# Optimization experiments

Hardware: AMD Instinct MI355X
Metric: run time of the kernel (lower is better)

Reference implementation:

```python
import jax, jax.numpy as jnp
import numpy as np

NH = 6
D = 78  # dim_k = dim_v, dk = dv = 13 per head
SCALE = 1.0 / np.sqrt(D // NH).astype(np.float32)


def _split(t):
    # (B, n, D) -> (B, H, n, dk)
    B, n, d = t.shape
    return t.reshape(B, n, NH, d // NH).transpose(0, 2, 1, 3)


def _merge(t):
    # (B, H, n, dk) -> (B, n, D)
    B, h, n, d = t.shape
    return t.transpose(0, 2, 1, 3).reshape(B, n, h * d)


def _cross_attn(x, y, Wq, Wk, Wv):
    # MultiHeadCrossSelfAttention / MultiHeadSelfAttention math (dropout=identity in eval;
    # attn_mask is expanded but never applied in the original forward).
    q = _split(x @ Wq)
    k = _split(y @ Wk)
    v = _split(y @ Wv)
    dist = jax.nn.softmax(jnp.einsum('bhqd,bhkd->bhqk', q, k) * SCALE, axis=-1)
    return _merge(jnp.einsum('bhqk,bhkd->bhqd', dist, v))


def _contrastive_attn(x, y, Wq, Wk, Wv):
    # MultiHeadContrastiveSelfAttention: softmax -> (1 - p) -> softmax -> matmul, residual q add.
    q = _split(x @ Wq)
    k = _split(y @ Wk)
    v = _split(y @ Wv)
    dist = jax.nn.softmax(jnp.einsum('bhqd,bhkd->bhqk', q, k) * SCALE, axis=-1)
    dist = jax.nn.softmax(1.0 - dist, axis=-1)
    return _merge(q + jnp.einsum('bhqk,bhkd->bhqd', dist, v))


def setup_inputs() -> dict:
    key = jax.random.key(0)
    ks = jax.random.split(key, 20)
    B, nT, nV, nA = 8, 1024, 1024, 1024
    inp = {
        'x': jax.random.normal(ks[0], (B, nT, D), jnp.float32),
        'y': jax.random.normal(ks[1], (B, nV, D), jnp.float32),
        'z': jax.random.normal(ks[2], (B, nA, D), jnp.float32),
        'mask_tv': jnp.zeros((B, nT, nV), jnp.bool_),
        'mask_ta': jnp.zeros((B, nT, nA), jnp.bool_),
    }
    names = ['Wq_tv', 'Wk_tv', 'Wv_tv', 'Wq_ta', 'Wk_ta', 'Wv_ta',
             'Wq_ctv', 'Wk_ctv', 'Wv_ctv', 'Wq_cta', 'Wk_cta', 'Wv_cta',
             'Wq_s', 'Wk_s', 'Wv_s']
    for i, nm in enumerate(names):
        inp[nm] = jax.random.normal(ks[3 + i], (D, D), jnp.float32) * 0.05
    return inp


def reference(x, y, z, mask_tv, mask_ta,
              Wq_tv, Wk_tv, Wv_tv, Wq_ta, Wk_ta, Wv_ta,
              Wq_ctv, Wk_ctv, Wv_ctv, Wq_cta, Wk_cta, Wv_cta,
              Wq_s, Wk_s, Wv_s):
    # masks are dead args in the original module (expanded but never applied)
    att_tv = _cross_attn(x, y, Wq_tv, Wk_tv, Wv_tv)          # MHSCA_TV
    att_ta = _cross_attn(x, z, Wq_ta, Wk_ta, Wv_ta)          # MHSCA_TA
    c_tv = _contrastive_attn(x, y, Wq_ctv, Wk_ctv, Wv_ctv)   # MHSCTA_TV
    c_ta = _contrastive_attn(x, z, Wq_cta, Wk_cta, Wv_cta)   # MHSCTA_TA
    # fuse three pooled modality tokens through the length-3 MHSA
    tokens = jnp.stack([x.mean(axis=1),
                        (att_tv + c_tv).mean(axis=1),
                        (att_ta + c_ta).mean(axis=1)], axis=1)  # (B, 3, D)
    fused = _cross_attn(tokens, tokens, Wq_s, Wk_s, Wv_s)       # MHSA
    # (B, 4*1024 + 3, D)
    return jnp.concatenate([att_tv, c_tv, att_ta, c_ta, fused], axis=1)
```

## Files before the change

### kernel.cpp

```cpp
#include <hip/hip_runtime.h>
#include <hip/hip_bf16.h>

#define BB 8
#define NN 1024
#define DM 78
#define NH 6
#define DK 13
#define NROW 4099
#define QSCL 0.40013158f
#define SCALE 0.27735009811261457f
#define INV1023 0.000977517106549365f

using bf16 = __hip_bfloat16;
typedef __attribute__((ext_vector_type(8))) short short8;
typedef __attribute__((ext_vector_type(4))) float f32x4;

#if __has_builtin(__builtin_amdgcn_exp2f)
#define EXP2(x) __builtin_amdgcn_exp2f(x)
#else
__device__ __forceinline__ float EXP2(float x) {
    float r;
    asm volatile("v_exp_f32 %0, %1\n\ts_nop 1" : "=v"(r) : "v"(x));
    return r;
}
#endif

#define MATSZ ((size_t)48 * 1024 * 16)

struct PW { const float* w[12]; };

__device__ __forceinline__ unsigned pkbf2(float a, float b) {
    __hip_bfloat162 t = __float22bfloat162_rn(make_float2(a, b));
    return *(unsigned*)&t;
}

__global__ __launch_bounds__(320) void proj_kernel(const float* __restrict__ x,
                                                   const float* __restrict__ y,
                                                   const float* __restrict__ z,
                                                   PW p,
                                                   unsigned* __restrict__ Qbf,
                                                   unsigned* __restrict__ Kbf,
                                                   unsigned* __restrict__ Vt,
                                                   float* __restrict__ Qf32,
                                                   float* __restrict__ sv,
                                                   float* __restrict__ tok) {
    __shared__ float AT[78 * 68];
    __shared__ float WL[78 * 80];
    int bid = blockIdx.x;
    int mat = bid >> 7;
    int rb = bid & 127;
    const float* src = (mat < 4) ? x : (((mat - 4) & 1) ? z : y);
    int tid = threadIdx.x;
    const float* sp = src + (size_t)rb * 64 * DM;
    for (int i = tid; i < 64 * DM; i += 320) {
        int r = i / DM, e = i - r * DM;
        AT[e * 68 + r] = sp[i];
    }
    const float* W = p.w[mat];
    for (int i = tid; i < DM * DM; i += 320) {
        int e = i / DM, c = i - e * DM;
        WL[e * 80 + c] = W[i];
    }
    __syncthreads();
    int rowg = tid / 20, colg = tid % 20;
    float acc[4][4] = {{0.f}};
    for (int e = 0; e < DM; ++e) {
        float4 a = *(const float4*)&AT[e * 68 + rowg * 4];
        float4 w = *(const float4*)&WL[e * 80 + colg * 4];
        acc[0][0] = fmaf(a.x, w.x, acc[0][0]); acc[0][1] = fmaf(a.x, w.y, acc[0][1]);
        acc[0][2] = fmaf(a.x, w.z, acc[0][2]); acc[0][3] = fmaf(a.x, w.w, acc[0][3]);
        acc[1][0] = fmaf(a.y, w.x, acc[1][0]); acc[1][1] = fmaf(a.y, w.y, acc[1][1]);
        acc[1][2] = fmaf(a.y, w.z, acc[1][2]); acc[1][3] = fmaf(a.y, w.w, acc[1][3]);
        acc[2][0] = fmaf(a.z, w.x, acc[2][0]); acc[2][1] = fmaf(a.z, w.y, acc[2][1]);
        acc[2][2] = fmaf(a.z, w.z, acc[2][2]); acc[2][3] = fmaf(a.z, w.w, acc[2][3]);
        acc[3][0] = fmaf(a.w, w.x, acc[3][0]); acc[3][1] = fmaf(a.w, w.y, acc[3][1]);
        acc[3][2] = fmaf(a.w, w.z, acc[3][2]); acc[3][3] = fmaf(a.w, w.w, acc[3][3]);
    }
    __syncthreads();
    float* CT = WL;
#pragma unroll
    for (int j = 0; j < 4; ++j)
#pragma unroll
        for (int k = 0; k < 4; ++k) {
            int c = colg * 4 + k;
            if (c < DM) CT[(rowg * 4 + j) * 81 + c] = acc[j][k];
        }
    __syncthreads();
    int bb = rb >> 4;
    int i0 = (rb & 15) * 64;
    if (mat < 8) {
        unsigned* dst = (mat < 4) ? Qbf : Kbf;
        int m4 = (mat < 4) ? mat : mat - 4;
        float scl = (mat < 4) ? QSCL : 1.0f;
        for (int t2 = tid; t2 < NH * 64 * 8; t2 += 320) {
            int hh = t2 >> 9;
            int rem = t2 & 511;
            int r = rem >> 3, cp = rem & 7;
            int c0 = cp * 2, c1 = cp * 2 + 1;
            float a = (c0 < DK) ? CT[r * 81 + hh * DK + c0] * scl : 0.f;
            float bv = (c1 < DK) ? CT[r * 81 + hh * DK + c1] * scl : 0.f;
            dst[(((size_t)m4 * 48 + bb * NH + hh) * 1024 + i0 + r) * 8 + cp] = pkbf2(a, bv);
        }
        if (mat >= 2) {
            for (int t2 = tid; t2 < 64 * DM; t2 += 320) {
                int r = t2 / DM, c = t2 - r * DM;
                int hh = c / DK, dd = c - hh * DK;
                Qf32[((size_t)(mat - 2) * 48 + bb * NH + hh) * 1024 * DK +
                     (size_t)(i0 + r) * DK + dd] = CT[r * 81 + c];
            }
        }
    } else {
        for (int t2 = tid; t2 < NH * 16 * 32; t2 += 320) {
            int hh = t2 >> 9;
            int rem = t2 & 511;
            int dd = rem >> 5, cp = rem & 31;
            float a, bv;
            if (dd < DK) {
                a = CT[(cp * 2) * 81 + hh * DK + dd];
                bv = CT[(cp * 2 + 1) * 81 + hh * DK + dd];
            } else if (dd == 13) { a = 1.f; bv = 1.f; }
            else { a = 0.f; bv = 0.f; }
            Vt[(((size_t)(mat - 8) * 48 + bb * NH + hh) * 16 + dd) * 512 +
               (i0 >> 1) + cp] = pkbf2(a, bv);
        }
        if (mat >= 10 && tid < DM) {
            int hh = tid / DK, dd = tid - hh * DK;
            float s = 0.f;
            for (int r = 0; r < 64; ++r) s += CT[r * 81 + tid];
            atomicAdd(&sv[((size_t)(mat - 10) * 48 + bb * NH + hh) * DK + dd], s);
        }
    }
    if (mat == 0 && tid < DM) {
        float s = 0.f;
        for (int r = 0; r < 64; ++r) s += AT[tid * 68 + r];
        atomicAdd(&tok[bb * DM + tid], s);
    }
}

__global__ __launch_bounds__(256) void att_kernel(const bf16* __restrict__ Qbf,
                                                  const bf16* __restrict__ Kbf,
                                                  const bf16* __restrict__ Vt,
                                                  const float* __restrict__ Qf32,
                                                  const float* __restrict__ sv,
                                                  float* __restrict__ tok,
                                                  float* __restrict__ out) {
    __shared__ short PL[4 * 2560];
    int bid = blockIdx.x;
    int qt = bid & 7;
    int rest = bid >> 3;
    int h = rest % NH; rest /= NH;
    int b = rest & 7;
    int g = rest >> 3;
    int tid = threadIdx.x, wave = tid >> 6, lane = tid & 63;
    int quad = lane >> 4, lq = lane & 15;
    size_t mb = (size_t)g * 48 + b * NH + h;
    int q0 = qt * 64 + wave * 16;
    int q1 = q0 + 512;

    short8 zero8 = {0, 0, 0, 0, 0, 0, 0, 0};
    short8 qfA = zero8, qfB = zero8;
    if (quad < 2) {
        qfA = *(const short8*)((const short*)Qbf + (mb * 1024 + q0 + lq) * 16 + quad * 8);
        qfB = *(const short8*)((const short*)Qbf + (mb * 1024 + q1 + lq) * 16 + quad * 8);
    }
    const short* Kp = (const short*)Kbf + mb * 1024 * 16;
    const short* Vp = (const short*)Vt + mb * 16 * 1024 + (size_t)lq * 1024;
    short* myP = &PL[wave * 2560];
    f32x4 OA = {0.f, 0.f, 0.f, 0.f};
    f32x4 OB = {0.f, 0.f, 0.f, 0.f};
    const f32x4 zz = {0.f, 0.f, 0.f, 0.f};

    short8 kX0 = zero8, kX1 = zero8, kY0 = zero8, kY1 = zero8, vX, vY;
    if (quad < 2) {
        kX0 = *(const short8*)(Kp + lq * 16 + quad * 8);
        kX1 = *(const short8*)(Kp + (16 + lq) * 16 + quad * 8);
        kY0 = *(const short8*)(Kp + (32 + lq) * 16 + quad * 8);
        kY1 = *(const short8*)(Kp + (48 + lq) * 16 + quad * 8);
    }
    vX = *(const short8*)(Vp + quad * 8);
    vY = *(const short8*)(Vp + 32 + quad * 8);

    for (int kt = 0; kt < 16; ++kt) {
        int nkey = kt * 64 + 64;
        f32x4 SX0 = __builtin_amdgcn_mfma_f32_16x16x32_bf16(kX0, qfA, zz, 0, 0, 0);
        f32x4 SX1 = __builtin_amdgcn_mfma_f32_16x16x32_bf16(kX1, qfA, zz, 0, 0, 0);
        f32x4 SX2 = __builtin_amdgcn_mfma_f32_16x16x32_bf16(kX0, qfB, zz, 0, 0, 0);
        f32x4 SX3 = __builtin_amdgcn_mfma_f32_16x16x32_bf16(kX1, qfB, zz, 0, 0, 0);
        f32x4 SY0 = __builtin_amdgcn_mfma_f32_16x16x32_bf16(kY0, qfA, zz, 0, 0, 0);
        f32x4 SY1 = __builtin_amdgcn_mfma_f32_16x16x32_bf16(kY1, qfA, zz, 0, 0, 0);
        f32x4 SY2 = __builtin_amdgcn_mfma_f32_16x16x32_bf16(kY0, qfB, zz, 0, 0, 0);
        f32x4 SY3 = __builtin_amdgcn_mfma_f32_16x16x32_bf16(kY1, qfB, zz, 0, 0, 0);
        short8 kX0n = zero8, kX1n = zero8, kY0n = zero8, kY1n = zero8, vXn, vYn;
        if (quad < 2) {
            kX0n = *(const short8*)(Kp + (nkey + lq) * 16 + quad * 8);
            kX1n = *(const short8*)(Kp + (nkey + 16 + lq) * 16 + quad * 8);
            kY0n = *(const short8*)(Kp + (nkey + 32 + lq) * 16 + quad * 8);
            kY1n = *(const short8*)(Kp + (nkey + 48 + lq) * 16 + quad * 8);
        }
        vXn = *(const short8*)(Vp + nkey + quad * 8);
        vYn = *(const short8*)(Vp + nkey + 32 + quad * 8);

        uint2 w0, w1;
        w0.x = pkbf2(EXP2(SX0[0]), EXP2(SX0[1]));
        w0.y = pkbf2(EXP2(SX0[2]), EXP2(SX0[3]));
        w1.x = pkbf2(EXP2(SX1[0]), EXP2(SX1[1]));
        w1.y = pkbf2(EXP2(SX1[2]), EXP2(SX1[3]));
        *(uint2*)(myP + lq * 40 + quad * 4) = w0;
        *(uint2*)(myP + lq * 40 + 16 + quad * 4) = w1;
        w0.x = pkbf2(EXP2(SX2[0]), EXP2(SX2[1]));
        w0.y = pkbf2(EXP2(SX2[2]), EXP2(SX2[3]));
        w1.x = pkbf2(EXP2(SX3[0]), EXP2(SX3[1]));
        w1.y = pkbf2(EXP2(SX3[2]), EXP2(SX3[3]));
        *(uint2*)(myP + 640 + lq * 40 + quad * 4) = w0;
        *(uint2*)(myP + 640 + lq * 40 + 16 + quad * 4) = w1;
        w0.x = pkbf2(EXP2(SY0[0]), EXP2(SY0[1]));
        w0.y = pkbf2(EXP2(SY0[2]), EXP2(SY0[3]));
        w1.x = pkbf2(EXP2(SY1[0]), EXP2(SY1[1]));
        w1.y = pkbf2(EXP2(SY1[2]), EXP2(SY1[3]));
        *(uint2*)(myP + 1280 + lq * 40 + quad * 4) = w0;
        *(uint2*)(myP + 1280 + lq * 40 + 16 + quad * 4) = w1;
        w0.x = pkbf2(EXP2(SY2[0]), EXP2(SY2[1]));
        w0.y = pkbf2(EXP2(SY2[2]), EXP2(SY2[3]));
        w1.x = pkbf2(EXP2(SY3[0]), EXP2(SY3[1]));
        w1.y = pkbf2(EXP2(SY3[2]), EXP2(SY3[3]));
        *(uint2*)(myP + 1920 + lq * 40 + quad * 4) = w0;
        *(uint2*)(myP + 1920 + lq * 40 + 16 + quad * 4) = w1;
        asm volatile("s_waitcnt lgkmcnt(0)" ::: "memory");
        short8 pXA = *(const short8*)(myP + lq * 40 + quad * 8);
        short8 pXB = *(const short8*)(myP + 640 + lq * 40 + quad * 8);
        short8 pYA = *(const short8*)(myP + 1280 + lq * 40 + quad * 8);
        short8 pYB = *(const short8*)(myP + 1920 + lq * 40 + quad * 8);
        OA = __builtin_amdgcn_mfma_f32_16x16x32_bf16(pXA, vX, OA, 0, 0, 0);
        OB = __builtin_amdgcn_mfma_f32_16x16x32_bf16(pXB, vX, OB, 0, 0, 0);
        OA = __builtin_amdgcn_mfma_f32_16x16x32_bf16(pYA, vY, OA, 0, 0, 0);
        OB = __builtin_amdgcn_mfma_f32_16x16x32_bf16(pYB, vY, OB, 0, 0, 0);
        kX0 = kX0n; kX1 = kX1n; kY0 = kY0n; kY1 = kY1n; vX = vXn; vY = vYn;
    }

    size_t rowbase = (g == 0) ? 0 : (g == 1 ? 2 * NN : (g == 2 ? NN : 3 * NN));
    float lA[4], lB[4];
#pragma unroll
    for (int r = 0; r < 4; ++r) {
        lA[r] = __shfl(OA[r], (lane & 48) | 13, 64);
        lB[r] = __shfl(OB[r], (lane & 48) | 13, 64);
    }
    float svv = 0.f;
    const float* qf32p = nullptr;
    if (g >= 2) {
        if (lq < DK) svv = sv[((size_t)(g - 2) * 48 + b * NH + h) * DK + lq];
        qf32p = Qf32 + ((size_t)(g - 2) * 48 + b * NH + h) * 1024 * DK + lq;
    }
    float vsum = 0.f;
#pragma unroll
    for (int r = 0; r < 4; ++r) {
        int mA = q0 + quad * 4 + r;
        int mB = q1 + quad * 4 + r;
        float A0 = OA[r] / lA[r];
        float A1 = OB[r] / lB[r];
        float v0, v1;
        if (g < 2) { v0 = A0; v1 = A1; }
        else {
            float qr0 = (lq < DK) ? qf32p[(size_t)mA * DK] : 0.f;
            float qr1 = (lq < DK) ? qf32p[(size_t)mB * DK] : 0.f;
            v0 = qr0 + (svv - A0) * INV1023;
            v1 = qr1 + (svv - A1) * INV1023;
        }
        if (lq < DK) {
            out[((size_t)b * NROW + rowbase + mA) * DM + h * DK + lq] = v0;
            out[((size_t)b * NROW + rowbase + mB) * DM + h * DK + lq] = v1;
            vsum += v0 + v1;
        }
    }
    vsum += __shfl_xor(vsum, 16);
    vsum += __shfl_xor(vsum, 32);
    if (quad == 0 && lq < DK) {
        int tki = (g & 1) ? 2 : 1;
        atomicAdd(&tok[(size_t)tki * (8 * DM) + b * DM + h * DK + lq], vsum);
    }
}

__global__ __launch_bounds__(256) void fused_kernel(const float* __restrict__ tok,
                                                    const float* __restrict__ Wq,
                                                    const float* __restrict__ Wk,
                                                    const float* __restrict__ Wv,
                                                    float* __restrict__ out) {
    __shared__ float T[3 * DM], Qs[3 * DM], Ks[3 * DM], Vs[3 * DM], P[NH * 9];
    int b = blockIdx.x, tid = threadIdx.x;
    if (tid < 234) {
        int t = tid / DM, d = tid - t * DM;
        T[tid] = tok[(size_t)t * (8 * DM) + b * DM + d] * (1.f / NN);
    }
    __syncthreads();
    for (int idx = tid; idx < 702; idx += 256) {
        int mat = idx / 234;
        int rem = idx - mat * 234;
        int t = rem / DM, d = rem - t * DM;
        const float* W = (mat == 0) ? Wq : (mat == 1 ? Wk : Wv);
        float a = 0.f;
        for (int e = 0; e < DM; ++e) a = fmaf(T[t * DM + e], W[(size_t)e * DM + d], a);
        float* dst = (mat == 0) ? Qs : (mat == 1 ? Ks : Vs);
        dst[t * DM + d] = a;
    }
    __syncthreads();
    if (tid < NH * 3) {
        int h = tid / 3, t = tid % 3;
        float s[3];
        for (int k = 0; k < 3; ++k) {
            float a = 0.f;
            for (int d2 = 0; d2 < DK; ++d2)
                a += Qs[t * DM + h * DK + d2] * Ks[k * DM + h * DK + d2];
            s[k] = a * SCALE;
        }
        float mm = fmaxf(s[0], fmaxf(s[1], s[2]));
        float e0 = __expf(s[0] - mm), e1 = __expf(s[1] - mm), e2 = __expf(s[2] - mm);
        float inv = 1.f / (e0 + e1 + e2);
        P[(h * 3 + t) * 3 + 0] = e0 * inv;
        P[(h * 3 + t) * 3 + 1] = e1 * inv;
        P[(h * 3 + t) * 3 + 2] = e2 * inv;
    }
    __syncthreads();
    if (tid < 234) {
        int t = tid / DM, d = tid - t * DM, h = d / DK;
        float a = 0.f;
        for (int k = 0; k < 3; ++k) a += P[(h * 3 + t) * 3 + k] * Vs[k * DM + d];
        out[((size_t)b * NROW + 4 * NN + t) * DM + d] = a;
    }
}

extern "C" void kernel_launch(void* const* d_in, const int* in_sizes, int n_in,
                              void* d_out, int out_size, void* d_ws, size_t ws_size,
                              hipStream_t stream) {
    const float* bigs[3] = {nullptr, nullptr, nullptr};
    const float* w[15];
    int nb = 0, nw = 0;
    for (int i = 0; i < n_in; ++i) {
        if (in_sizes[i] == BB * NN * DM && nb < 3) bigs[nb++] = (const float*)d_in[i];
        else if (in_sizes[i] == DM * DM && nw < 15) w[nw++] = (const float*)d_in[i];
    }
    if (nb < 3 || nw < 15) {
        bigs[0] = (const float*)d_in[0]; bigs[1] = (const float*)d_in[1];
        bigs[2] = (const float*)d_in[2];
        int base = (n_in >= 20) ? 5 : 3;
        for (int i = 0; i < 15; ++i) w[i] = (const float*)d_in[base + i];
    }
    const float* x = bigs[0];
    const float* y = bigs[1];
    const float* z = bigs[2];
    float* out = (float*)d_out;

    bf16* Qbf = (bf16*)d_ws;
    bf16* Kbf = Qbf + 4 * MATSZ;
    bf16* Vt  = Kbf + 4 * MATSZ;
    float* Qf32 = (float*)(Vt + 4 * MATSZ);
    float* sv = Qf32 + (size_t)2 * 48 * 1024 * DK;
    float* tok = sv + 2 * 48 * DK;

    PW pp;
    const float* wsel[12] = {w[0], w[3], w[6], w[9],
                             w[1], w[4], w[7], w[10],
                             w[2], w[5], w[8], w[11]};
    for (int i = 0; i < 12; ++i) pp.w[i] = wsel[i];

    hipMemsetAsync(sv, 0, (2 * 48 * DK + 3 * 8 * DM) * sizeof(float), stream);
    proj_kernel<<<1536, 320, 0, stream>>>(x, y, z, pp, (unsigned*)Qbf, (unsigned*)Kbf,
                                          (unsigned*)Vt, Qf32, sv, tok);
    att_kernel<<<4 * BB * NH * 8, 256, 0, stream>>>(Qbf, Kbf, Vt, Qf32, sv, tok, out);
    fused_kernel<<<BB, 256, 0, stream>>>(tok, w[12], w[13], w[14], out);
}
```

Measured before the change: 220.8 us.

## Use bf16 MFMA for projections whose outputs are stored as bf16

The projection kernel is split into two paths. Blocks whose outputs are consumed only as bf16 (Q for the plain cross attention, K, V) now run a bf16 MFMA 16x16x32 GEMM on padded LDS tiles. The contrastive Q projections, which also need fp32 output for the residual add, keep an FP32 FMA path that now uses 256 threads and loads K in two chunks to shrink LDS. The aim is to cut projection compute time and LDS footprint so more blocks fit per CU, at the cost of bf16 input rounding in the GEMM and more complex block remapping.

```diff
diff --git a/kernel.cpp b/kernel.cpp
--- a/kernel.cpp
+++ b/kernel.cpp
@@ -34,7 +34,7 @@
     return *(unsigned*)&t;
 }
 
-__global__ __launch_bounds__(320) void proj_kernel(const float* __restrict__ x,
+__global__ __launch_bounds__(256) void proj_kernel(const float* __restrict__ x,
                                                    const float* __restrict__ y,
                                                    const float* __restrict__ z,
                                                    PW p,
@@ -44,96 +44,172 @@
                                                    float* __restrict__ Qf32,
                                                    float* __restrict__ sv,
                                                    float* __restrict__ tok) {
-    __shared__ float AT[78 * 68];
-    __shared__ float WL[78 * 80];
+    __shared__ unsigned SMEM[7488];
     int bid = blockIdx.x;
-    int mat = bid >> 7;
-    int rb = bid & 127;
+    int tid = threadIdx.x;
+    int mat, rb;
+    if (bid < 256) { mat = 2 + (bid >> 7); rb = bid & 127; }
+    else {
+        int t = bid - 256;
+        int midx = t >> 7;
+        mat = (midx < 2) ? midx : midx + 2;
+        rb = t & 127;
+    }
     const float* src = (mat < 4) ? x : (((mat - 4) & 1) ? z : y);
-    int tid = threadIdx.x;
     const float* sp = src + (size_t)rb * 64 * DM;
-    for (int i = tid; i < 64 * DM; i += 320) {
-        int r = i / DM, e = i - r * DM;
-        AT[e * 68 + r] = sp[i];
-    }
     const float* W = p.w[mat];
-    for (int i = tid; i < DM * DM; i += 320) {
-        int e = i / DM, c = i - e * DM;
-        WL[e * 80 + c] = W[i];
-    }
-    __syncthreads();
-    int rowg = tid / 20, colg = tid % 20;
-    float acc[4][4] = {{0.f}};
-    for (int e = 0; e < DM; ++e) {
-        float4 a = *(const float4*)&AT[e * 68 + rowg * 4];
-        float4 w = *(const float4*)&WL[e * 80 + colg * 4];
-        acc[0][0] = fmaf(a.x, w.x, acc[0][0]); acc[0][1] = fmaf(a.x, w.y, acc[0][1]);
-        acc[0][2] = fmaf(a.x, w.z, acc[0][2]); acc[0][3] = fmaf(a.x, w.w, acc[0][3]);
-        acc[1][0] = fmaf(a.y, w.x, acc[1][0]); acc[1][1] = fmaf(a.y, w.y, acc[1][1]);
-        acc[1][2] = fmaf(a.y, w.z, acc[1][2]); acc[1][3] = fmaf(a.y, w.w, acc[1][3]);
-        acc[2][0] = fmaf(a.z, w.x, acc[2][0]); acc[2][1] = fmaf(a.z, w.y, acc[2][1]);
-        acc[2][2] = fmaf(a.z, w.z, acc[2][2]); acc[2][3] = fmaf(a.z, w.w, acc[2][3]);
-        acc[3][0] = fmaf(a.w, w.x, acc[3][0]); acc[3][1] = fmaf(a.w, w.y, acc[3][1]);
-        acc[3][2] = fmaf(a.w, w.z, acc[3][2]); acc[3][3] = fmaf(a.w, w.w, acc[3][3]);
-    }
-    __syncthreads();
-    float* CT = WL;
-#pragma unroll
-    for (int j = 0; j < 4; ++j)
-#pragma unroll
-        for (int k = 0; k < 4; ++k) {
-            int c = colg * 4 + k;
-            if (c < DM) CT[(rowg * 4 + j) * 81 + c] = acc[j][k];
-        }
-    __syncthreads();
     int bb = rb >> 4;
     int i0 = (rb & 15) * 64;
-    if (mat < 8) {
-        unsigned* dst = (mat < 4) ? Qbf : Kbf;
-        int m4 = (mat < 4) ? mat : mat - 4;
-        float scl = (mat < 4) ? QSCL : 1.0f;
-        for (int t2 = tid; t2 < NH * 64 * 8; t2 += 320) {
+    float* CT = (float*)SMEM;
+
+    if (bid < 256) {
+        float* AT = (float*)SMEM;
+        float* WL = AT + 39 * 68;
+        int rowg = tid >> 4, colg = tid & 15;
+        float acc[4][5] = {{0.f}};
+        for (int ch = 0; ch < 2; ++ch) {
+            int e0 = ch * 39;
+            if (ch) __syncthreads();
+            for (int i = tid; i < 64 * 39; i += 256) {
+                int r = i / 39, er = i - r * 39;
+                AT[er * 68 + r] = sp[r * DM + e0 + er];
+            }
+            for (int i = tid; i < 39 * 80; i += 256) {
+                int er = i / 80, c = i - er * 80;
+                WL[er * 80 + c] = (c < DM) ? W[(size_t)(e0 + er) * DM + c] : 0.f;
+            }
+            __syncthreads();
+            if (mat == 2 && tid < 39) {
+                float s = 0.f;
+                for (int r = 0; r < 64; ++r) s += AT[tid * 68 + r];
+                atomicAdd(&tok[bb * DM + e0 + tid], s);
+            }
+            for (int er = 0; er < 39; ++er) {
+                float4 a4 = *(const float4*)&AT[er * 68 + rowg * 4];
+                float av[4] = {a4.x, a4.y, a4.z, a4.w};
+                const float* wr = &WL[er * 80 + colg * 5];
+                float w0 = wr[0], w1 = wr[1], w2 = wr[2], w3 = wr[3], w4 = wr[4];
+#pragma unroll
+                for (int j = 0; j < 4; ++j) {
+                    acc[j][0] = fmaf(av[j], w0, acc[j][0]);
+                    acc[j][1] = fmaf(av[j], w1, acc[j][1]);
+                    acc[j][2] = fmaf(av[j], w2, acc[j][2]);
+                    acc[j][3] = fmaf(av[j], w3, acc[j][3]);
+                    acc[j][4] = fmaf(av[j], w4, acc[j][4]);
+                }
+            }
+        }
+        __syncthreads();
+#pragma unroll
+        for (int j = 0; j < 4; ++j)
+#pragma unroll
+            for (int k = 0; k < 5; ++k) {
+                int c = colg * 5 + k;
+                if (c < DM) CT[(rowg * 4 + j) * 81 + c] = acc[j][k];
+            }
+        __syncthreads();
+        for (int t2 = tid; t2 < NH * 64 * 8; t2 += 256) {
             int hh = t2 >> 9;
             int rem = t2 & 511;
             int r = rem >> 3, cp = rem & 7;
             int c0 = cp * 2, c1 = cp * 2 + 1;
-            float a = (c0 < DK) ? CT[r * 81 + hh * DK + c0] * scl : 0.f;
-            float bv = (c1 < DK) ? CT[r * 81 + hh * DK + c1] * scl : 0.f;
-            dst[(((size_t)m4 * 48 + bb * NH + hh) * 1024 + i0 + r) * 8 + cp] = pkbf2(a, bv);
-        }
-        if (mat >= 2) {
-            for (int t2 = tid; t2 < 64 * DM; t2 += 320) {
-                int r = t2 / DM, c = t2 - r * DM;
-                int hh = c / DK, dd = c - hh * DK;
-                Qf32[((size_t)(mat - 2) * 48 + bb * NH + hh) * 1024 * DK +
-                     (size_t)(i0 + r) * DK + dd] = CT[r * 81 + c];
-            }
+            float a = (c0 < DK) ? CT[r * 81 + hh * DK + c0] * QSCL : 0.f;
+            float bv = (c1 < DK) ? CT[r * 81 + hh * DK + c1] * QSCL : 0.f;
+            Qbf[(((size_t)mat * 48 + bb * NH + hh) * 1024 + i0 + r) * 8 + cp] = pkbf2(a, bv);
+        }
+        for (int t2 = tid; t2 < 64 * DM; t2 += 256) {
+            int r = t2 / DM, c = t2 - r * DM;
+            int hh = c / DK, dd = c - hh * DK;
+            Qf32[((size_t)(mat - 2) * 48 + bb * NH + hh) * 1024 * DK +
+                 (size_t)(i0 + r) * DK + dd] = CT[r * 81 + c];
         }
     } else {
-        for (int t2 = tid; t2 < NH * 16 * 32; t2 += 320) {
-            int hh = t2 >> 9;
-            int rem = t2 & 511;
-            int dd = rem >> 5, cp = rem & 31;
-            float a, bv;
-            if (dd < DK) {
-                a = CT[(cp * 2) * 81 + hh * DK + dd];
-                bv = CT[(cp * 2 + 1) * 81 + hh * DK + dd];
-            } else if (dd == 13) { a = 1.f; bv = 1.f; }
-            else { a = 0.f; bv = 0.f; }
-            Vt[(((size_t)(mat - 8) * 48 + bb * NH + hh) * 16 + dd) * 512 +
-               (i0 >> 1) + cp] = pkbf2(a, bv);
-        }
-        if (mat >= 10 && tid < DM) {
-            int hh = tid / DK, dd = tid - hh * DK;
-            float s = 0.f;
-            for (int r = 0; r < 64; ++r) s += CT[r * 81 + tid];
-            atomicAdd(&sv[((size_t)(mat - 10) * 48 + bb * NH + hh) * DK + dd], s);
-        }
-    }
-    if (mat == 0 && tid < DM) {
-        float s = 0.f;
-        for (int r = 0; r < 64; ++r) s += AT[tid * 68 + r];
-        atomicAdd(&tok[bb * DM + tid], s);
+        unsigned* ALu = SMEM;
+        unsigned* WTu = SMEM + 64 * 52;
+        const float2* sp2 = (const float2*)sp;
+        for (int i = tid; i < 64 * 39; i += 256) {
+            float2 f2 = sp2[i];
+            int r = i / 39, pc = i - r * 39;
+            ALu[r * 52 + pc] = pkbf2(f2.x, f2.y);
+        }
+        for (int i = tid; i < 64 * 13; i += 256) {
+            int r = i / 13, pc = i - r * 13;
+            ALu[r * 52 + 39 + pc] = 0u;
+        }
+        for (int i = tid; i < 80 * 52; i += 256) {
+            int n = i / 52, pc = i - n * 52;
+            int k0 = pc * 2;
+            float a = (n < DM && k0 < DM) ? W[(size_t)k0 * DM + n] : 0.f;
+            float bv = (n < DM && k0 + 1 < DM) ? W[(size_t)(k0 + 1) * DM + n] : 0.f;
+            WTu[i] = pkbf2(a, bv);
+        }
+        __syncthreads();
+        int wv = tid >> 6, lane = tid & 63, quad = lane >> 4, lq = lane & 15;
+        int r0 = wv * 16;
+        const short* ALs = (const short*)ALu;
+        const short* WTs = (const short*)WTu;
+        short8 af0 = *(const short8*)(ALs + (r0 + lq) * 104 + quad * 8);
+        short8 af1 = *(const short8*)(ALs + (r0 + lq) * 104 + 32 + quad * 8);
+        short8 af2 = *(const short8*)(ALs + (r0 + lq) * 104 + 64 + quad * 8);
+        const f32x4 zz = {0.f, 0.f, 0.f, 0.f};
+        f32x4 acc[5];
+#pragma unroll
+        for (int n = 0; n < 5; ++n) acc[n] = zz;
+#pragma unroll
+        for (int n = 0; n < 5; ++n) {
+            const short* wb = WTs + (n * 16 + lq) * 104 + quad * 8;
+            acc[n] = __builtin_amdgcn_mfma_f32_16x16x32_bf16(
+                af0, *(const short8*)wb, acc[n], 0, 0, 0);
+            acc[n] = __builtin_amdgcn_mfma_f32_16x16x32_bf16(
+                af1, *(const short8*)(wb + 32), acc[n], 0, 0, 0);
+            acc[n] = __builtin_amdgcn_mfma_f32_16x16x32_bf16(
+                af2, *(const short8*)(wb + 64), acc[n], 0, 0, 0);
+        }
+        __syncthreads();
+#pragma unroll
+        for (int n = 0; n < 5; ++n) {
+            int c = n * 16 + lq;
+            if (c < DM) {
+#pragma unroll
+                for (int r = 0; r < 4; ++r)
+                    CT[(r0 + quad * 4 + r) * 81 + c] = acc[n][r];
+            }
+        }
+        __syncthreads();
+        if (mat < 8) {
+            unsigned* dst = (mat < 4) ? Qbf : Kbf;
+            int m4 = (mat < 4) ? mat : mat - 4;
+            float scl = (mat < 4) ? QSCL : 1.0f;
+            for (int t2 = tid; t2 < NH * 64 * 8; t2 += 256) {
+                int hh = t2 >> 9;
+                int rem = t2 & 511;
+                int r = rem >> 3, cp = rem & 7;
+                int c0 = cp * 2, c1 = cp * 2 + 1;
+                float a = (c0 < DK) ? CT[r * 81 + hh * DK + c0] * scl : 0.f;
+                float bv = (c1 < DK) ? CT[r * 81 + hh * DK + c1] * scl : 0.f;
+                dst[(((size_t)m4 * 48 + bb * NH + hh) * 1024 + i0 + r) * 8 + cp] = pkbf2(a, bv);
+            }
+        } else {
+            for (int t2 = tid; t2 < NH * 16 * 32; t2 += 256) {
+                int hh = t2 >> 9;
+                int rem = t2 & 511;
+                int dd = rem >> 5, cp = rem & 31;
+                float a, bv;
+                if (dd < DK) {
+                    a = CT[(cp * 2) * 81 + hh * DK + dd];
+                    bv = CT[(cp * 2 + 1) * 81 + hh * DK + dd];
+                } else if (dd == 13) { a = 1.f; bv = 1.f; }
+                else { a = 0.f; bv = 0.f; }
+                Vt[(((size_t)(mat - 8) * 48 + bb * NH + hh) * 16 + dd) * 512 +
+                   (i0 >> 1) + cp] = pkbf2(a, bv);
+            }
+            if (mat >= 10 && tid < DM) {
+                int hh = tid / DK, dd = tid - hh * DK;
+                float s = 0.f;
+                for (int r = 0; r < 64; ++r) s += CT[r * 81 + tid];
+                atomicAdd(&sv[((size_t)(mat - 10) * 48 + bb * NH + hh) * DK + dd], s);
+            }
+        }
     }
 }
 
@@ -362,7 +438,7 @@
     for (int i = 0; i < 12; ++i) pp.w[i] = wsel[i];
 
     hipMemsetAsync(sv, 0, (2 * 48 * DK + 3 * 8 * DM) * sizeof(float), stream);
-    proj_kernel<<<1536, 320, 0, stream>>>(x, y, z, pp, (unsigned*)Qbf, (unsigned*)Kbf,
+    proj_kernel<<<1536, 256, 0, stream>>>(x, y, z, pp, (unsigned*)Qbf, (unsigned*)Kbf,
                                           (unsigned*)Vt, Qf32, sv, tok);
     att_kernel<<<4 * BB * NH * 8, 256, 0, stream>>>(Qbf, Kbf, Vt, Qf32, sv, tok, out);
     fused_kernel<<<BB, 256, 0, stream>>>(tok, w[12], w[13], w[14], out);
```

Result: faster. 215.9 us (-2.2%).
